# Performance work log

Hardware: AMD Instinct MI355X
Metric: run time of the kernel (lower is better)

The kernel has to match this reference:

```python
import jax, jax.numpy as jnp
import numpy as np
from itertools import combinations

# Factor-graph structure exactly as in generate_graph / generate_h_cord / generate_g_cord (N = 15)
N = 15
D = 128            # NDIM
E = 16             # edge feature dim (fc_edge output)
CN2 = N * (N - 1) // 2            # 105 pair z-nodes / h-factors
CN3 = N * (N - 1) * (N - 2) // 6  # 455 triangle g-factors
NV = N + CN2                      # 120 variable nodes (persons + pair z-nodes)
B = 64


def _build_structure():
    h_id = {c: i + N for i, c in enumerate(combinations(range(N), 2))}
    G = [[] for _ in range(N + N * (N - 1) + CN3)]
    hidx = N + CN2
    for u in range(N):
        for v in range(u + 1, N):
            G[hidx].extend([u, v, h_id[(u, v)]])
            G[u].append(hidx)
            G[v].append(hidx)
            G[h_id[(u, v)]].append(hidx)
            hidx += 1
    gidx = N + N * (N - 1)
    for i in range(N):
        for j in range(i + 1, N):
            for k in range(j + 1, N):
                z1, z2, z3 = h_id[(i, j)], h_id[(i, k)], h_id[(j, k)]
                G[gidx].extend([z1, z2, z3])
                G[z1].append(gidx)
                G[z2].append(gidx)
                G[z3].append(gidx)
                gidx += 1
    deg = max(3, N - 1)  # 14
    for l in G:
        while len(l) < deg:
            l.append(l[-1])
    graph = np.array(G, dtype=np.int32)  # [680, 14]
    h_cord = np.array([[u, v, i + N] for i, (u, v) in enumerate(combinations(range(N), 2))], dtype=np.int32)  # [105, 3]
    g_cord = np.array(
        [[h_id[(i, j)], h_id[(i, k)], h_id[(j, k)]]
         for i in range(N) for j in range(i + 1, N) for k in range(j + 1, N)], dtype=np.int32)  # [455, 3]
    return graph, h_cord, g_cord


GRAPH_NP, H_CORD_NP, G_CORD_NP = _build_structure()
DEG = GRAPH_NP.shape[1]  # 14
NG = GRAPH_NP.shape[0]   # 680


def setup_inputs() -> dict:
    key = jax.random.key(0)
    k1, k2 = jax.random.split(key)
    node_feats = jax.random.normal(k1, (B, NV, D), dtype=jnp.float32)
    W_edge = jax.random.normal(k2, (2 * D, E), dtype=jnp.float32) * (2.0 / (2 * D)) ** 0.5  # kaiming
    b_edge = jnp.zeros((E,), dtype=jnp.float32)
    return {"node_feats": node_feats, "W_edge": W_edge, "b_edge": b_edge}


def reference(node_feats, W_edge, b_edge):
    graph = jnp.asarray(GRAPH_NP)
    h_cord = jnp.asarray(H_CORD_NP)
    g_cord = jnp.asarray(G_CORD_NP)

    def single(vf):  # vf: [NV, D] variable-node features (persons + pair z-nodes)
        hf = vf[h_cord].mean(axis=1)   # [105, D] h-factor feats: mean over (u, v, z_uv)
        gf = vf[g_cord].mean(axis=1)   # [455, D] g-factor feats: mean over (z1, z2, z3)
        nff = jnp.concatenate([vf, hf, gf], axis=0)  # [680, D] all graph-node feats
        # edge features: concat(self feat repeated over neighbors, gathered neighbor feats)
        self_rep = jnp.broadcast_to(nff[:, None, :], (NG, DEG, D))
        ef = jnp.concatenate([self_rep, nff[graph]], axis=-1)  # [680, 14, 2D]
        msg = jax.nn.relu(ef @ W_edge + b_edge)  # per-edge MLP -> [680, 14, 16]
        return msg.mean(axis=1)  # mean-pool over incident edges -> [680, 16]

    return jax.vmap(single)(node_feats)  # [B, 680, 16]
```

## Files before the change

### kernel.cpp

```cpp
#include <hip/hip_runtime.h>

#define NGRAPH 680

__device__ __forceinline__ int pair_index(int a, int b) {
    return a * (29 - a) / 2 + (b - a - 1);
}

struct PairTab { unsigned char u[105]; unsigned char v[105]; };
__device__ constexpr PairTab make_pair_tab() {
    PairTab t{};
    int f = 0;
    for (int a = 0; a < 15; a++)
        for (int b = a + 1; b < 15; b++) { t.u[f] = (unsigned char)a; t.v[f] = (unsigned char)b; f++; }
    return t;
}
__device__ constexpr PairTab PAIRS = make_pair_tab();

struct TriTab { unsigned char z1[455]; unsigned char z2[455]; unsigned char z3[455]; };
__device__ constexpr TriTab make_tri_tab() {
    TriTab t{};
    int n = 0;
    for (int i = 0; i < 15; i++)
        for (int j = i + 1; j < 15; j++)
            for (int k = j + 1; k < 15; k++) {
                t.z1[n] = (unsigned char)(15 + i * (29 - i) / 2 + (j - i - 1));
                t.z2[n] = (unsigned char)(15 + i * (29 - i) / 2 + (k - i - 1));
                t.z3[n] = (unsigned char)(15 + j * (29 - j) / 2 + (k - j - 1));
                n++;
            }
    return t;
}
__device__ constexpr TriTab TRI = make_tri_tab();

__global__ __launch_bounds__(512) void fgnn_fused(
    const float* __restrict__ vf,
    const float* __restrict__ W,
    const float* __restrict__ bias,
    float* __restrict__ out)
{
    __shared__ float Wl[128][4];
    __shared__ float Ps[120][2];
    __shared__ float Pt[120][2];
    __shared__ float TH[105][2];

    const int tid = threadIdx.x;
    const int s   = blockIdx.x >> 6;
    const int b   = blockIdx.x & 63;
    const int c0  = s * 2;

    if (tid < 128) {
        float2 ws = *(const float2*)(W + tid * 16 + c0);
        float2 wt = *(const float2*)(W + (128 + tid) * 16 + c0);
        Wl[tid][0] = ws.x; Wl[tid][1] = ws.y;
        Wl[tid][2] = wt.x; Wl[tid][3] = wt.y;
    }
    __syncthreads();

    if (tid < 240) {
        const int r = tid >> 1;
        const int g = tid & 1;
        const float4* va   = (const float4*)(vf + ((size_t)b * 120 + r) * 128);
        const float2* wcol = (const float2*)&Wl[0][g * 2];
        float a0 = 0.f, a1 = 0.f;
        #pragma unroll
        for (int k4 = 0; k4 < 32; k4++) {
            float4 a  = va[k4];
            float2 w0 = wcol[(4 * k4 + 0) * 2];
            float2 w1 = wcol[(4 * k4 + 1) * 2];
            float2 w2 = wcol[(4 * k4 + 2) * 2];
            float2 w3 = wcol[(4 * k4 + 3) * 2];
            a0 = fmaf(a.x, w0.x, a0); a1 = fmaf(a.x, w0.y, a1);
            a0 = fmaf(a.y, w1.x, a0); a1 = fmaf(a.y, w1.y, a1);
            a0 = fmaf(a.z, w2.x, a0); a1 = fmaf(a.z, w2.y, a1);
            a0 = fmaf(a.w, w3.x, a0); a1 = fmaf(a.w, w3.y, a1);
        }
        if (g == 0) {
            Ps[r][0] = a0 + bias[c0];
            Ps[r][1] = a1 + bias[c0 + 1];
        } else {
            Pt[r][0] = a0;
            Pt[r][1] = a1;
        }
    }
    __syncthreads();

    if (tid < 210) {
        int f = tid >> 1, c = tid & 1;
        TH[f][c] = (Pt[PAIRS.u[f]][c] + Pt[PAIRS.v[f]][c] + Pt[15 + f][c]) * (1.0f / 3.0f);
    }
    __syncthreads();

    const float inv3  = 1.0f / 3.0f;
    const float inv14 = 1.0f / 14.0f;
    float* outb = out + (size_t)b * NGRAPH * 16 + c0;

    for (int i = tid; i < NGRAPH; i += 512) {
        float r0, r1;
        if (i < 15) {
            float s0 = Ps[i][0], s1 = Ps[i][1];
            float acc0 = 0.f, acc1 = 0.f;
            #pragma unroll
            for (int v2 = 0; v2 < 15; v2++) {
                if (v2 == i) continue;
                int f = pair_index(min(i, v2), max(i, v2));
                acc0 += fmaxf(s0 + TH[f][0], 0.f);
                acc1 += fmaxf(s1 + TH[f][1], 0.f);
            }
            r0 = acc0 * inv14; r1 = acc1 * inv14;
        } else if (i < 120) {
            int f = i - 15;
            int u = PAIRS.u[f], v = PAIRS.v[f];
            float s0 = Ps[i][0], s1 = Ps[i][1];
            float t0 = Pt[i][0], t1 = Pt[i][1];
            float acc0 = fmaxf(s0 + TH[f][0], 0.f);
            float acc1 = fmaxf(s1 + TH[f][1], 0.f);
            #pragma unroll
            for (int w = 0; w < 15; w++) {
                if (w == u || w == v) continue;
                int zuw = 15 + pair_index(min(u, w), max(u, w));
                int zvw = 15 + pair_index(min(v, w), max(v, w));
                acc0 += fmaxf(s0 + (t0 + Pt[zuw][0] + Pt[zvw][0]) * inv3, 0.f);
                acc1 += fmaxf(s1 + (t1 + Pt[zuw][1] + Pt[zvw][1]) * inv3, 0.f);
            }
            r0 = acc0 * inv14; r1 = acc1 * inv14;
        } else if (i < 225) {
            int f = i - 120;
            int u = PAIRS.u[f], v = PAIRS.v[f], z = 15 + f;
            float S0 = (Ps[u][0] + Ps[v][0] + Ps[z][0]) * inv3;
            float S1 = (Ps[u][1] + Ps[v][1] + Ps[z][1]) * inv3;
            r0 = (fmaxf(S0 + Pt[u][0], 0.f) + fmaxf(S0 + Pt[v][0], 0.f)
                + 12.f * fmaxf(S0 + Pt[z][0], 0.f)) * inv14;
            r1 = (fmaxf(S1 + Pt[u][1], 0.f) + fmaxf(S1 + Pt[v][1], 0.f)
                + 12.f * fmaxf(S1 + Pt[z][1], 0.f)) * inv14;
        } else {
            int t3 = i - 225;
            int z1 = TRI.z1[t3], z2 = TRI.z2[t3], z3 = TRI.z3[t3];
            float S0 = (Ps[z1][0] + Ps[z2][0] + Ps[z3][0]) * inv3;
            float S1 = (Ps[z1][1] + Ps[z2][1] + Ps[z3][1]) * inv3;
            r0 = (fmaxf(S0 + Pt[z1][0], 0.f) + fmaxf(S0 + Pt[z2][0], 0.f)
                + 12.f * fmaxf(S0 + Pt[z3][0], 0.f)) * inv14;
            r1 = (fmaxf(S1 + Pt[z1][1], 0.f) + fmaxf(S1 + Pt[z2][1], 0.f)
                + 12.f * fmaxf(S1 + Pt[z3][1], 0.f)) * inv14;
        }
        *(float2*)(outb + (size_t)i * 16) = make_float2(r0, r1);
    }
}

extern "C" void kernel_launch(void* const* d_in, const int* in_sizes, int n_in,
                              void* d_out, int out_size, void* d_ws, size_t ws_size,
                              hipStream_t stream) {
    const float* vf   = (const float*)d_in[0];
    const float* W    = (const float*)d_in[1];
    const float* bias = (const float*)d_in[2];
    float* o = (float*)d_out;

    fgnn_fused<<<512, 512, 0, stream>>>(vf, W, bias, o);
}
```

Before: 14.53 us.

## Split projection K-dimension across four wavegroups and read weights via scalar loads

Removes the shared-memory staging of the weight slice and its barrier. Each 128-thread group now handles one half of K for either the source or target projection, with the weight index made wave-uniform through readfirstlane so weights can be fetched with scalar loads. Partial sums are reduced through a new shared buffer. This uses all 512 threads instead of 240 and shortens the serial dot-product chain, at the cost of an extra reduction step and barrier.

```diff
diff --git a/kernel.cpp b/kernel.cpp
--- a/kernel.cpp
+++ b/kernel.cpp
@@ -38,7 +38,7 @@
     const float* __restrict__ bias,
     float* __restrict__ out)
 {
-    __shared__ float Wl[128][4];
+    __shared__ float Pp[2][120][2];
     __shared__ float Ps[120][2];
     __shared__ float Pt[120][2];
     __shared__ float TH[105][2];
@@ -48,32 +48,34 @@
     const int b   = blockIdx.x & 63;
     const int c0  = s * 2;
 
-    if (tid < 128) {
-        float2 ws = *(const float2*)(W + tid * 16 + c0);
-        float2 wt = *(const float2*)(W + (128 + tid) * 16 + c0);
-        Wl[tid][0] = ws.x; Wl[tid][1] = ws.y;
-        Wl[tid][2] = wt.x; Wl[tid][3] = wt.y;
-    }
-    __syncthreads();
+    const int r  = tid & 127;
+    const int gk = __builtin_amdgcn_readfirstlane(tid >> 7);
+    const int kh = gk & 1;
+    const int g  = gk >> 1;
 
-    if (tid < 240) {
-        const int r = tid >> 1;
-        const int g = tid & 1;
-        const float4* va   = (const float4*)(vf + ((size_t)b * 120 + r) * 128);
-        const float2* wcol = (const float2*)&Wl[0][g * 2];
-        float a0 = 0.f, a1 = 0.f;
+    float a0 = 0.f, a1 = 0.f;
+    if (r < 120) {
+        const float4* va = (const float4*)(vf + ((size_t)b * 120 + r) * 128 + kh * 64);
+        const float*  Wg = W + g * 2048 + kh * 1024 + c0;
         #pragma unroll
-        for (int k4 = 0; k4 < 32; k4++) {
+        for (int k4 = 0; k4 < 16; k4++) {
             float4 a  = va[k4];
-            float2 w0 = wcol[(4 * k4 + 0) * 2];
-            float2 w1 = wcol[(4 * k4 + 1) * 2];
-            float2 w2 = wcol[(4 * k4 + 2) * 2];
-            float2 w3 = wcol[(4 * k4 + 3) * 2];
+            float2 w0 = *(const float2*)(Wg + (4 * k4 + 0) * 16);
+            float2 w1 = *(const float2*)(Wg + (4 * k4 + 1) * 16);
+            float2 w2 = *(const float2*)(Wg + (4 * k4 + 2) * 16);
+            float2 w3 = *(const float2*)(Wg + (4 * k4 + 3) * 16);
             a0 = fmaf(a.x, w0.x, a0); a1 = fmaf(a.x, w0.y, a1);
             a0 = fmaf(a.y, w1.x, a0); a1 = fmaf(a.y, w1.y, a1);
             a0 = fmaf(a.z, w2.x, a0); a1 = fmaf(a.z, w2.y, a1);
             a0 = fmaf(a.w, w3.x, a0); a1 = fmaf(a.w, w3.y, a1);
         }
+        if (kh == 1) { Pp[g][r][0] = a0; Pp[g][r][1] = a1; }
+    }
+    __syncthreads();
+
+    if (r < 120 && kh == 0) {
+        a0 += Pp[g][r][0];
+        a1 += Pp[g][r][1];
         if (g == 0) {
             Ps[r][0] = a0 + bias[c0];
             Ps[r][1] = a1 + bias[c0 + 1];
```

After: 17.62 us. +21.2%, slower.
